# Optimization experiments

Hardware: AMD Instinct MI355X
Metric: run time of the kernel (lower is better)

Reference implementation:

```python
import jax, jax.numpy as jnp
import numpy as np

B, S, D, E, L = 4, 384, 300, 50, 2
HD = D // L  # head_dim = 150


def _linear_params(k, fin, fout):
    bnd = 1.0 / np.sqrt(fin)
    kw, kb = jax.random.split(k)
    W = jax.random.uniform(kw, (fout, fin), minval=-bnd, maxval=bnd, dtype=jnp.float32)
    b = jax.random.uniform(kb, (fout,), minval=-bnd, maxval=bnd, dtype=jnp.float32)
    return W, b


def setup_inputs() -> dict:
    key = jax.random.key(0)
    ks = jax.random.split(key, 6)
    W0, b0 = _linear_params(ks[0], D, HD)            # weight_list[0]: Linear(300, 150)
    W1, b1 = _linear_params(ks[1], D + HD, HD)       # weight_list[1]: Linear(450, 150)
    Wh, bh = _linear_params(ks[2], 2 * HD + E, E)    # Edgeupdate.W: Linear(350, 50)
    Wout, bout = _linear_params(ks[3], D, D)         # linear_output: Linear(300, 300)
    adj = jax.random.uniform(ks[4], (B, S, S, E), dtype=jnp.float32)
    gcn_inputs = jax.random.normal(ks[5], (B, S, D), dtype=jnp.float32)
    return dict(adj=adj, gcn_inputs=gcn_inputs, W0=W0, b0=b0, W1=W1, b1=b1,
                Wh=Wh, bh=bh, Wout=Wout, bout=bout)


def reference(adj, gcn_inputs, W0, b0, W1, b1, Wh, bh, Wout, bout):
    # Edgeupdate weight split: cat order is [edge(E), node1(HD), node2(HD)]
    Wh_e = Wh[:, :E]            # [E, E]
    Wh_1 = Wh[:, E:E + HD]      # [E, HD]
    Wh_2 = Wh[:, E + HD:]       # [E, HD]

    outputs = gcn_inputs        # [B, S, D]
    cache = [gcn_inputs]
    out_list = []
    for (Wl, bl) in ((W0, b0), (W1, b1)):
        e_dim = adj.shape[-1]
        # mean over edge channels of (adj_e @ outputs): einsum fuses the mean
        Ax = jnp.einsum('bike,bkd->bid', adj, outputs) / e_dim   # [B, S, din]
        # AxW = W_l(Ax) + W_l(outputs)  (same linear applied twice, bias twice)
        AxW = (Ax @ Wl.T + bl) + (outputs @ Wl.T + bl)           # [B, S, HD]
        gAxW = jax.nn.relu(AxW)
        # Edgeupdate highway: new_edge[b,i,j] = W([edge[b,i,j]; g[b,j]; g[b,i]]) + bh
        # (node1[b,i,j] = g[b,j], node2[b,i,j] = g[b,i] from the expand/permute)
        edge_part = adj @ Wh_e.T                                  # [B, S, S, E]
        n1 = gAxW @ Wh_1.T                                        # [B, S, E]
        n2 = gAxW @ Wh_2.T                                        # [B, S, E]
        adj = edge_part + n1[:, None, :, :] + n2[:, :, None, :] + bh
        cache.append(gAxW)
        outputs = jnp.concatenate(cache, axis=2)                  # growing concat
        out_list.append(gAxW)  # gcn_drop is identity in eval mode

    gcn_outputs = jnp.concatenate(out_list, axis=2) + gcn_inputs  # [B, S, D]
    return gcn_outputs @ Wout.T + bout
```

## Files before the change

### kernel.cpp

```cpp
#include <hip/hip_runtime.h>

constexpr int Bc  = 4;
constexpr int Sc  = 384;
constexpr int Dc  = 300;
constexpr int Ec  = 50;
constexpr int HDc = 150;
constexpr int WHC = 350;
constexpr int MT  = Bc * Sc;

typedef __attribute__((ext_vector_type(8))) short bf16x8;
typedef __attribute__((ext_vector_type(4))) float f32x4;

__device__ __forceinline__ short f2bf(float x) {
    union { float f; unsigned u; } v; v.f = x;
    unsigned r = (v.u + 0x7FFFu + ((v.u >> 16) & 1u)) >> 16;
    return (short)r;
}

__device__ __forceinline__ void s12_unit(const float* __restrict__ G,
                                         const float* __restrict__ sm,
                                         float* __restrict__ s12, int unit)
{
    int wave = threadIdx.x >> 6, lane = threadIdx.x & 63;
    int g = unit * 4 + wave;
    const float* gp = G + (long)g * Dc;
    float a = 0.f, c = 0.f;
    #pragma unroll
    for (int h0 = 0; h0 < HDc; h0 += 64) {
        int h = h0 + lane;
        if (h < HDc) { float v = gp[h]; a += v * sm[64 + h]; c += v * sm[224 + h]; }
    }
    #pragma unroll
    for (int off = 32; off; off >>= 1) {
        a += __shfl_down(a, off);
        c += __shfl_down(c, off);
    }
    if (lane == 0) { s12[2*g] = a; s12[2*g + 1] = c; }
}

template<int BSRC, int A1M, int HASD, int HASB, int RELU, int PRE>
__device__ __forceinline__ void mgemm_body(
    short* As, short* Bs, int bx, int by, int b,
    const float* __restrict__ A, int lda, long sA,
    const float* __restrict__ Bw, int ldb, long sB,
    const float* __restrict__ W1a, const float* __restrict__ WoutP,
    const float* __restrict__ Dm, int ldd, long sD,
    const float* __restrict__ bias, float bscale,
    const float* __restrict__ s12, const float* __restrict__ sm,
    float* __restrict__ C, int ldc, long sC,
    int M, int N, int K)
{
    const float* Ap = A + (long)b * sA;
    const float* Bp = Bw + (long)b * sB;
    const float* Dp = Dm + (long)b * sD;
    float* Cp = C + (long)b * sC;

    const int tid  = threadIdx.x;
    const int wave = tid >> 6, lane = tid & 63;
    const int wm = wave & 1, wn = wave >> 1;
    const int lm = lane & 15, quad = lane >> 4;
    const int m0 = by * 32, n0 = bx * 32;

    const int srow = tid >> 3;
    const int sk   = (tid & 7) * 8;
    const int nc   = tid & 31;
    const int kr   = tid >> 5;

    float sbh = 0.f; const float* s1p = nullptr; float s2v = 0.f;
    if constexpr (A1M) {
        sbh = sm[384];
        s1p = s12 + 2L * Sc * b;
        s2v = s1p[2 * (m0 + srow) + 1];
    }

    const int cn = n0 + wn * 16 + lm;
    float bpre = 0.f;
    float dpre[4] = {0.f, 0.f, 0.f, 0.f};
    if constexpr (PRE) {
        if constexpr (HASB) { if (cn < N) bpre = bias[cn]; }
        if constexpr (HASD) {
            #pragma unroll
            for (int r = 0; r < 4; ++r) {
                int cm = m0 + wm * 16 + quad * 4 + r;
                if (cn < N && cm < M) dpre[r] = Dp[(long)cm * ldd + cn];
            }
        }
    }

    float ra[8], rb[8];

    auto stageA = [&](int k0) {
        int am = m0 + srow;
        int kb = k0 + sk;
        if constexpr (A1M) {
            float4 u = *(const float4*)(Ap + (long)am * lda + kb);
            float4 w = *(const float4*)(Ap + (long)am * lda + kb + 4);
            const float* up = (const float*)&u;
            const float* wp = (const float*)&w;
            #pragma unroll
            for (int j = 0; j < 4; ++j) {
                ra[j]     = (up[j] + s1p[2*(kb + j)]     + s2v + sbh) * (1.0f/Ec);
                ra[4 + j] = (wp[j] + s1p[2*(kb + 4 + j)] + s2v + sbh) * (1.0f/Ec);
            }
        } else {
            if (kb + 7 < K) {
                float4 u = *(const float4*)(Ap + (long)am * lda + kb);
                float4 w = *(const float4*)(Ap + (long)am * lda + kb + 4);
                ra[0]=u.x; ra[1]=u.y; ra[2]=u.z; ra[3]=u.w;
                ra[4]=w.x; ra[5]=w.y; ra[6]=w.z; ra[7]=w.w;
            } else {
                #pragma unroll
                for (int j = 0; j < 8; ++j) {
                    int k = kb + j;
                    ra[j] = (k < K) ? Ap[(long)am * lda + k] : 0.f;
                }
            }
        }
    };

    auto stageB = [&](int k0) {
        if constexpr (BSRC == 0) {
            int n = n0 + nc;
            bool nok = n < N;
            #pragma unroll
            for (int p = 0; p < 8; ++p) {
                int k = k0 + kr + p * 8;
                rb[p] = nok ? Bp[(long)k * ldb + n] : 0.f;
            }
        } else {
            int nr = n0 + srow;
            bool nok = nr < N;
            const float* wp = Bp; int ld = ldb; int nn = nr;
            if constexpr (BSRC == 2) {
                if (nr < 150)      { wp = Bp;    ld = 300; nn = nr; }
                else if (nr < 300) { wp = W1a;   ld = 450; nn = nr - 150; }
                else               { wp = WoutP; ld = 300; nn = nr - 300; }
            }
            #pragma unroll
            for (int p = 0; p < 4; ++p) {
                int k = k0 + sk + 2 * p;
                if (nok && k + 1 < K) {
                    float2 v = *(const float2*)(wp + (long)nn * ld + k);
                    rb[2*p] = v.x; rb[2*p + 1] = v.y;
                } else {
                    rb[2*p]     = (nok && k < K)     ? wp[(long)nn * ld + k]     : 0.f;
                    rb[2*p + 1] = (nok && k + 1 < K) ? wp[(long)nn * ld + k + 1] : 0.f;
                }
            }
        }
    };

    auto stash = [&]() {
        #pragma unroll
        for (int j = 0; j < 8; ++j) As[srow * 72 + sk + j] = f2bf(ra[j]);
        if constexpr (BSRC == 0) {
            #pragma unroll
            for (int p = 0; p < 8; ++p) Bs[nc * 72 + kr + p * 8] = f2bf(rb[p]);
        } else {
            #pragma unroll
            for (int j = 0; j < 8; ++j) Bs[srow * 72 + sk + j] = f2bf(rb[j]);
        }
    };

    f32x4 acc = {0.f, 0.f, 0.f, 0.f};

    stageA(0); stageB(0);
    for (int k0 = 0; k0 < K; k0 += 64) {
        __syncthreads();
        stash();
        __syncthreads();
        if (k0 + 64 < K) { stageA(k0 + 64); stageB(k0 + 64); }
        {
            bf16x8 a0 = *(const bf16x8*)(As + (wm*16 + lm) * 72 + quad * 8);
            bf16x8 b0 = *(const bf16x8*)(Bs + (wn*16 + lm) * 72 + quad * 8);
            acc = __builtin_amdgcn_mfma_f32_16x16x32_bf16(a0, b0, acc, 0, 0, 0);
            bf16x8 a1 = *(const bf16x8*)(As + (wm*16 + lm) * 72 + 32 + quad * 8);
            bf16x8 b1 = *(const bf16x8*)(Bs + (wn*16 + lm) * 72 + 32 + quad * 8);
            acc = __builtin_amdgcn_mfma_f32_16x16x32_bf16(a1, b1, acc, 0, 0, 0);
        }
    }

    if (cn < N) {
        #pragma unroll
        for (int r = 0; r < 4; ++r) {
            int cm = m0 + wm * 16 + quad * 4 + r;
            if (cm < M) {
                float v = acc[r];
                if constexpr (HASD) v += PRE ? dpre[r] : Dp[(long)cm * ldd + cn];
                if constexpr (HASB) v += bscale * (PRE ? bpre : bias[cn]);
                if constexpr (RELU) v = fmaxf(v, 0.f);
                Cp[(long)cm * ldc + cn] = v;
            }
        }
    }
}

template<int BSRC, int A1M, int HASD, int HASB, int RELU>
__global__ __launch_bounds__(256)
void mgemm(const float* __restrict__ A, int lda, long sA,
           const float* __restrict__ Bw, int ldb, long sB,
           const float* __restrict__ W1a, const float* __restrict__ WoutP,
           const float* __restrict__ Dm, int ldd, long sD,
           const float* __restrict__ bias, float bscale,
           const float* __restrict__ s12, const float* __restrict__ sm,
           float* __restrict__ C, int ldc, long sC,
           int M, int N, int K)
{
    __shared__ short As[32 * 72];
    __shared__ short Bs[32 * 72];
    mgemm_body<BSRC,A1M,HASD,HASB,RELU,1>(As, Bs,
        blockIdx.x, blockIdx.y, blockIdx.z,
        A, lda, sA, Bw, ldb, sB, W1a, WoutP, Dm, ldd, sD,
        bias, bscale, s12, sm, C, ldc, sC, M, N, K);
}

__global__ __launch_bounds__(256)
void fused1(const float* __restrict__ adj, const float* __restrict__ X,
            const float* __restrict__ W0, const float* __restrict__ W1,
            const float* __restrict__ Wout, const float* __restrict__ Wh,
            const float* __restrict__ bh,
            float* __restrict__ sm, float* __restrict__ A0,
            float* __restrict__ wadj, float* __restrict__ R)
{
    __shared__ float lds[64 * 51 + 64];
    const int bx = blockIdx.x, t = threadIdx.x;

    if (bx < 912) {
        short* As = (short*)lds;
        short* Bs = As + 32 * 72;
        mgemm_body<2,0,0,0,0,0>(As, Bs, bx % 19, bx / 19, 0,
            X, Dc, 0, W0, 300, 0, W1, Wout,
            nullptr, 0, 0, nullptr, 0.f, nullptr, nullptr,
            R, 600, 0, MT, 600, Dc);
    } else if (bx == 912) {
        for (int u = t; u < 512; u += 256) {
            if (u < Ec) {
                float s = 0.f;
                for (int e = 0; e < Ec; ++e) s += Wh[e*WHC + u];
                sm[u] = s;
            } else if (u >= 64 && u < 64 + HDc) {
                int h = u - 64; float s = 0.f;
                for (int e = 0; e < Ec; ++e) s += Wh[e*WHC + Ec + h];
                sm[u] = s;
            } else if (u >= 224 && u < 224 + HDc) {
                int h = u - 224; float s = 0.f;
                for (int e = 0; e < Ec; ++e) s += Wh[e*WHC + Ec + HDc + h];
                sm[u] = s;
            } else if (u == 384) {
                float s = 0.f;
                for (int e = 0; e < Ec; ++e) s += bh[e];
                sm[u] = s;
            }
        }
    } else {
        const int unit = bx - 913;
        float* tile = lds;
        float* wec  = lds + 64 * 51;

        long base = (long)unit * 3200;
        const float4* p4 = (const float4*)(adj + base);
        float4 v0 = p4[t];
        float4 v1 = p4[t + 256];
        float4 v2 = p4[t + 512];
        float4 v3 = {0.f, 0.f, 0.f, 0.f};
        if (t < 32) v3 = p4[t + 768];

        if (t < Ec) {
            float s = 0.f;
            for (int e = 0; e < Ec; ++e) s += Wh[e * WHC + t];
            wec[t] = s;
        }

        auto scat = [&](int i, const float4& v) {
            const float* vp = (const float*)&v;
            #pragma unroll
            for (int j = 0; j < 4; ++j) {
                int e = 4 * i + j;
                tile[(e / 50) * 51 + (e % 50)] = vp[j];
            }
        };
        scat(t, v0);
        scat(t + 256, v1);
        scat(t + 512, v2);
        if (t < 32) scat(t + 768, v3);
        __syncthreads();

        int r = t >> 2, q = t & 3;
        int h0 = q * 13, h1 = (q == 3) ? 50 : h0 + 13;
        const float* row = tile + r * 51;
        float s = 0.f, w = 0.f;
        for (int i = h0; i < h1; ++i) { float v = row[i]; s += v; w += v * wec[i]; }
        s += __shfl_xor(s, 1); w += __shfl_xor(w, 1);
        s += __shfl_xor(s, 2); w += __shfl_xor(w, 2);
        if (q == 0) {
            int g = unit * 64 + r;
            A0[g]   = s * (1.0f / Ec);
            wadj[g] = w;
        }
    }
}

__global__ __launch_bounds__(256)
void fused3(const float* __restrict__ Gbuf, const float* __restrict__ sm,
            float* __restrict__ s12, const float* __restrict__ W1,
            float* __restrict__ R, const float* __restrict__ Wout,
            const float* __restrict__ bout, float* __restrict__ out)
{
    __shared__ short As[32 * 72];
    __shared__ short Bs[32 * 72];
    const int bx = blockIdx.x;

    if (bx < 480) {
        mgemm_body<1,0,1,1,0,1>(As, Bs, bx % 10, bx / 10, 0,
            Gbuf, Dc, 0, Wout, Dc, 0, nullptr, nullptr,
            R + 2 * HDc, 600, 0, bout, 1.0f, nullptr, nullptr,
            out, Dc, 0, MT, Dc, HDc);
    } else if (bx < 480 + 240) {
        int v = bx - 480;
        mgemm_body<1,0,1,0,0,1>(As, Bs, v % 5, v / 5, 0,
            Gbuf, Dc, 0, W1 + Dc, Dc + HDc, 0, nullptr, nullptr,
            R + HDc, 600, 0, nullptr, 0.f, nullptr, nullptr,
            R + HDc, 600, 0, MT, HDc, HDc);
    } else {
        s12_unit(Gbuf, sm, s12, bx - 720);
    }
}

extern "C" void kernel_launch(void* const* d_in, const int* in_sizes, int n_in,
                              void* d_out, int out_size, void* d_ws, size_t ws_size,
                              hipStream_t stream) {
    const float* adj  = (const float*)d_in[0];
    const float* X    = (const float*)d_in[1];
    const float* W0   = (const float*)d_in[2];
    const float* b0   = (const float*)d_in[3];
    const float* W1   = (const float*)d_in[4];
    const float* b1   = (const float*)d_in[5];
    const float* Wh   = (const float*)d_in[6];
    const float* bh   = (const float*)d_in[7];
    const float* Wout = (const float*)d_in[8];
    const float* bout = (const float*)d_in[9];
    float* out = (float*)d_out;

    float* ws   = (float*)d_ws;
    float* sm   = ws;
    float* A0   = sm + 512;
    float* wadj = A0 + Bc * Sc * Sc;
    float* R    = wadj + Bc * Sc * Sc;
    float* Gbuf = R + (long)Bc * Sc * 600;
    float* s12  = Gbuf + (long)Bc * Sc * Dc;

    const long AS = (long)Sc * Sc;
    const long RS = (long)Sc * 600;
    const long GS = (long)Sc * Dc;

    fused1<<<912 + 1 + (Bc*Sc*Sc)/64, 256, 0, stream>>>(
        adj, X, W0, W1, Wout, Wh, bh, sm, A0, wadj, R);

    mgemm<0,0,1,1,1><<<dim3(5, 12, Bc), 256, 0, stream>>>(
        A0, Sc, AS, R, 600, RS, nullptr, nullptr,
        R, 600, RS, b0, 2.0f, nullptr, nullptr,
        Gbuf, Dc, GS, Sc, HDc, Sc);

    fused3<<<480 + 240 + 384, 256, 0, stream>>>(
        Gbuf, sm, s12, W1, R, Wout, bout, out);

    mgemm<0,1,1,1,1><<<dim3(5, 12, Bc), 256, 0, stream>>>(
        wadj, Sc, AS, R + HDc, 600, RS, nullptr, nullptr,
        R + HDc, 600, RS, b1, 2.0f, s12, sm,
        Gbuf + HDc, Dc, GS, Sc, HDc, Sc);

    mgemm<1,0,1,0,0><<<dim3(10, 48, 1), 256, 0, stream>>>(
        Gbuf + HDc, Dc, 0, Wout + HDc, Dc, 0, nullptr, nullptr,
        out, Dc, 0, nullptr, 0.f, nullptr, nullptr,
        out, Dc, 0, MT, Dc, HDc);
}
```

Measured before the change: 225.9 us.

## Fuse per-layer aggregation, projection and output GEMMs into row-block kernels

Replaces the four post-setup launches (two batched aggregation GEMMs, a mixed fused3 kernel, and an output GEMM) with two kernels. Each block of 32 rows runs the full layer chain in shared memory: the adjacency aggregation, then the ReLU node features kept in LDS as bf16, then the s12 edge scalars, the W1 projection and the Wout contribution. The second kernel also applies the s12/bias edge correction while staging the A tile. This removes launches and the Gbuf round trips through global memory. The cost is only 48 blocks on a many-CU GPU, heavy register and LDS use, and serial work inside each block, so low occupancy could outweigh the savings.

```diff
diff --git a/kernel.cpp b/kernel.cpp
--- a/kernel.cpp
+++ b/kernel.cpp
@@ -17,25 +17,9 @@
     return (short)r;
 }
 
-__device__ __forceinline__ void s12_unit(const float* __restrict__ G,
-                                         const float* __restrict__ sm,
-                                         float* __restrict__ s12, int unit)
-{
-    int wave = threadIdx.x >> 6, lane = threadIdx.x & 63;
-    int g = unit * 4 + wave;
-    const float* gp = G + (long)g * Dc;
-    float a = 0.f, c = 0.f;
-    #pragma unroll
-    for (int h0 = 0; h0 < HDc; h0 += 64) {
-        int h = h0 + lane;
-        if (h < HDc) { float v = gp[h]; a += v * sm[64 + h]; c += v * sm[224 + h]; }
-    }
-    #pragma unroll
-    for (int off = 32; off; off >>= 1) {
-        a += __shfl_down(a, off);
-        c += __shfl_down(c, off);
-    }
-    if (lane == 0) { s12[2*g] = a; s12[2*g + 1] = c; }
+__device__ __forceinline__ float bf2f(short s) {
+    union { unsigned u; float f; } v; v.u = ((unsigned)(unsigned short)s) << 16;
+    return v.f;
 }
 
 template<int BSRC, int A1M, int HASD, int HASB, int RELU, int PRE>
@@ -193,25 +177,6 @@
             }
         }
     }
-}
-
-template<int BSRC, int A1M, int HASD, int HASB, int RELU>
-__global__ __launch_bounds__(256)
-void mgemm(const float* __restrict__ A, int lda, long sA,
-           const float* __restrict__ Bw, int ldb, long sB,
-           const float* __restrict__ W1a, const float* __restrict__ WoutP,
-           const float* __restrict__ Dm, int ldd, long sD,
-           const float* __restrict__ bias, float bscale,
-           const float* __restrict__ s12, const float* __restrict__ sm,
-           float* __restrict__ C, int ldc, long sC,
-           int M, int N, int K)
-{
-    __shared__ short As[32 * 72];
-    __shared__ short Bs[32 * 72];
-    mgemm_body<BSRC,A1M,HASD,HASB,RELU,1>(As, Bs,
-        blockIdx.x, blockIdx.y, blockIdx.z,
-        A, lda, sA, Bw, ldb, sB, W1a, WoutP, Dm, ldd, sD,
-        bias, bscale, s12, sm, C, ldc, sC, M, N, K);
 }
 
 __global__ __launch_bounds__(256)
@@ -301,28 +266,368 @@
 }
 
 __global__ __launch_bounds__(256)
-void fused3(const float* __restrict__ Gbuf, const float* __restrict__ sm,
-            float* __restrict__ s12, const float* __restrict__ W1,
-            float* __restrict__ R, const float* __restrict__ Wout,
-            const float* __restrict__ bout, float* __restrict__ out)
+void fused23(const float* __restrict__ A0, float* __restrict__ R,
+             const float* __restrict__ W1, const float* __restrict__ Wout,
+             const float* __restrict__ b0v, const float* __restrict__ boutv,
+             const float* __restrict__ smv, float* __restrict__ s12,
+             float* __restrict__ out)
 {
-    __shared__ short As[32 * 72];
-    __shared__ short Bs[32 * 72];
-    const int bx = blockIdx.x;
-
-    if (bx < 480) {
-        mgemm_body<1,0,1,1,0,1>(As, Bs, bx % 10, bx / 10, 0,
-            Gbuf, Dc, 0, Wout, Dc, 0, nullptr, nullptr,
-            R + 2 * HDc, 600, 0, bout, 1.0f, nullptr, nullptr,
-            out, Dc, 0, MT, Dc, HDc);
-    } else if (bx < 480 + 240) {
-        int v = bx - 480;
-        mgemm_body<1,0,1,0,0,1>(As, Bs, v % 5, v / 5, 0,
-            Gbuf, Dc, 0, W1 + Dc, Dc + HDc, 0, nullptr, nullptr,
-            R + HDc, 600, 0, nullptr, 0.f, nullptr, nullptr,
-            R + HDc, 600, 0, MT, HDc, HDc);
-    } else {
-        s12_unit(Gbuf, sm, s12, bx - 720);
+    __shared__ short A6[6 * 2304];
+    __shared__ short Bs5[5 * 2304];
+    __shared__ short Gs[3 * 2304];
+
+    const int tid  = threadIdx.x;
+    const int wave = tid >> 6, lane = tid & 63;
+    const int wm = wave & 1, wn = wave >> 1;
+    const int lm = lane & 15, quad = lane >> 4;
+    const int srow = tid >> 3, sk = (tid & 7) * 8;
+    const int nc = tid & 31, kr = tid >> 5;
+    const int cml = wm * 16 + quad * 4;
+
+    const int b  = blockIdx.x / 12;
+    const int m0 = (blockIdx.x % 12) * 32;
+    const int gm0 = b * Sc + m0;
+    const float* Ap = A0 + (long)b * (Sc * Sc);
+    const float* Pp = R  + (long)b * (Sc * 600);
+
+    for (int i = tid; i < 3 * 2304; i += 256) Gs[i] = 0;
+
+    #pragma unroll
+    for (int c = 0; c < 6; ++c) {
+        const float* ap = Ap + (long)(m0 + srow) * Sc + c * 64 + sk;
+        float4 u = *(const float4*)ap;
+        float4 w = *(const float4*)(ap + 4);
+        short* d = A6 + c * 2304 + srow * 72 + sk;
+        d[0]=f2bf(u.x); d[1]=f2bf(u.y); d[2]=f2bf(u.z); d[3]=f2bf(u.w);
+        d[4]=f2bf(w.x); d[5]=f2bf(w.y); d[6]=f2bf(w.z); d[7]=f2bf(w.w);
+    }
+
+    float dpre[5][4], b0pre[5];
+    #pragma unroll
+    for (int nt = 0; nt < 5; ++nt) {
+        int cn = nt * 32 + wn * 16 + lm;
+        b0pre[nt] = (cn < 150) ? b0v[cn] : 0.f;
+        #pragma unroll
+        for (int r = 0; r < 4; ++r)
+            dpre[nt][r] = (cn < 150) ? Pp[(long)(m0 + cml + r) * 600 + cn] : 0.f;
+    }
+
+    float rbs[5][8];
+    f32x4 acc[5];
+    const f32x4 fz = {0.f, 0.f, 0.f, 0.f};
+
+    auto stageB_P = [&](int k0) {
+        #pragma unroll
+        for (int nt = 0; nt < 5; ++nt) {
+            int n = nt * 32 + nc; bool nok = n < 150;
+            #pragma unroll
+            for (int p = 0; p < 8; ++p)
+                rbs[nt][p] = nok ? Pp[(long)(k0 + kr + p * 8) * 600 + n] : 0.f;
+        }
+    };
+    auto stashB_k = [&]() {
+        #pragma unroll
+        for (int nt = 0; nt < 5; ++nt)
+            #pragma unroll
+            for (int p = 0; p < 8; ++p)
+                Bs5[nt * 2304 + nc * 72 + kr + p * 8] = f2bf(rbs[nt][p]);
+    };
+    auto stageB_W = [&](const float* Wbase, int ldw, int nbase, int nlim,
+                        int klim, int k0) {
+        #pragma unroll
+        for (int nt = 0; nt < 5; ++nt) {
+            int nr = nbase + nt * 32 + srow; bool nok = nr < nlim;
+            const float* wp = Wbase + (long)nr * ldw;
+            #pragma unroll
+            for (int p = 0; p < 4; ++p) {
+                int k = k0 + sk + 2 * p;
+                rbs[nt][2*p]   = (nok && k     < klim) ? wp[k]     : 0.f;
+                rbs[nt][2*p+1] = (nok && k + 1 < klim) ? wp[k + 1] : 0.f;
+            }
+        }
+    };
+    auto stashB_r = [&]() {
+        #pragma unroll
+        for (int nt = 0; nt < 5; ++nt)
+            #pragma unroll
+            for (int j = 0; j < 8; ++j)
+                Bs5[nt * 2304 + srow * 72 + sk + j] = f2bf(rbs[nt][j]);
+    };
+    auto mfma5 = [&](const short* Abase, int ki) {
+        const short* Af = Abase + ki * 2304 + (wm * 16 + lm) * 72;
+        bf16x8 a0 = *(const bf16x8*)(Af + quad * 8);
+        bf16x8 a1 = *(const bf16x8*)(Af + 32 + quad * 8);
+        #pragma unroll
+        for (int nt = 0; nt < 5; ++nt) {
+            const short* Bf = Bs5 + nt * 2304 + (wn * 16 + lm) * 72;
+            acc[nt] = __builtin_amdgcn_mfma_f32_16x16x32_bf16(
+                a0, *(const bf16x8*)(Bf + quad * 8), acc[nt], 0, 0, 0);
+            acc[nt] = __builtin_amdgcn_mfma_f32_16x16x32_bf16(
+                a1, *(const bf16x8*)(Bf + 32 + quad * 8), acc[nt], 0, 0, 0);
+        }
+    };
+
+    #pragma unroll
+    for (int nt = 0; nt < 5; ++nt) acc[nt] = fz;
+    stageB_P(0);
+    for (int ki = 0; ki < 6; ++ki) {
+        __syncthreads();
+        stashB_k();
+        __syncthreads();
+        if (ki < 5) stageB_P((ki + 1) * 64);
+        mfma5(A6, ki);
+    }
+    #pragma unroll
+    for (int nt = 0; nt < 5; ++nt) {
+        int cn = nt * 32 + wn * 16 + lm;
+        if (cn < 150) {
+            #pragma unroll
+            for (int r = 0; r < 4; ++r) {
+                float g = fmaxf(acc[nt][r] + dpre[nt][r] + 2.f * b0pre[nt], 0.f);
+                Gs[(cn >> 6) * 2304 + (cml + r) * 72 + (cn & 63)] = f2bf(g);
+            }
+        }
+    }
+    __syncthreads();
+
+    float dq[5][4];
+    #pragma unroll
+    for (int nt = 0; nt < 5; ++nt) {
+        int cn = nt * 32 + wn * 16 + lm;
+        #pragma unroll
+        for (int r = 0; r < 4; ++r)
+            dq[nt][r] = (cn < 150) ? Pp[(long)(m0 + cml + r) * 600 + 150 + cn] : 0.f;
+    }
+
+    {
+        int row = tid >> 3, p = tid & 7;
+        int c0 = p * 19, c1 = (c0 + 19 < 150) ? c0 + 19 : 150;
+        float a = 0.f, c2 = 0.f;
+        for (int c = c0; c < c1; ++c) {
+            float g = bf2f(Gs[(c >> 6) * 2304 + row * 72 + (c & 63)]);
+            a  += g * smv[64 + c];
+            c2 += g * smv[224 + c];
+        }
+        a += __shfl_xor(a, 1);  c2 += __shfl_xor(c2, 1);
+        a += __shfl_xor(a, 2);  c2 += __shfl_xor(c2, 2);
+        a += __shfl_xor(a, 4);  c2 += __shfl_xor(c2, 4);
+        if (p == 0) { s12[2 * (gm0 + row)] = a; s12[2 * (gm0 + row) + 1] = c2; }
+    }
+
+    #pragma unroll
+    for (int nt = 0; nt < 5; ++nt) acc[nt] = fz;
+    stageB_W(W1 + Dc, 450, 0, 150, 150, 0);
+    for (int ki = 0; ki < 3; ++ki) {
+        __syncthreads();
+        stashB_r();
+        __syncthreads();
+        if (ki < 2) stageB_W(W1 + Dc, 450, 0, 150, 150, (ki + 1) * 64);
+        mfma5(Gs, ki);
+    }
+    #pragma unroll
+    for (int nt = 0; nt < 5; ++nt) {
+        int cn = nt * 32 + wn * 16 + lm;
+        if (cn < 150) {
+            #pragma unroll
+            for (int r = 0; r < 4; ++r)
+                R[(long)(gm0 + cml + r) * 600 + 150 + cn] = acc[nt][r] + dq[nt][r];
+        }
+    }
+
+    #pragma unroll
+    for (int g = 0; g < 2; ++g) {
+        float d3[5][4], bop[5];
+        #pragma unroll
+        for (int nt = 0; nt < 5; ++nt) {
+            int cn = (g * 5 + nt) * 32 + wn * 16 + lm;
+            bop[nt] = (cn < 300) ? boutv[cn] : 0.f;
+            #pragma unroll
+            for (int r = 0; r < 4; ++r)
+                d3[nt][r] = (cn < 300) ? R[(long)(gm0 + cml + r) * 600 + 300 + cn] : 0.f;
+        }
+        #pragma unroll
+        for (int nt = 0; nt < 5; ++nt) acc[nt] = fz;
+        stageB_W(Wout, 300, g * 160, 300, 150, 0);
+        for (int ki = 0; ki < 3; ++ki) {
+            __syncthreads();
+            stashB_r();
+            __syncthreads();
+            if (ki < 2) stageB_W(Wout, 300, g * 160, 300, 150, (ki + 1) * 64);
+            mfma5(Gs, ki);
+        }
+        #pragma unroll
+        for (int nt = 0; nt < 5; ++nt) {
+            int cn = (g * 5 + nt) * 32 + wn * 16 + lm;
+            if (cn < 300) {
+                #pragma unroll
+                for (int r = 0; r < 4; ++r)
+                    out[(long)(gm0 + cml + r) * 300 + cn] = acc[nt][r] + d3[nt][r] + bop[nt];
+            }
+        }
+    }
+}
+
+__global__ __launch_bounds__(256)
+void fused45(const float* __restrict__ wadj, float* __restrict__ R,
+             const float* __restrict__ b1v, const float* __restrict__ Wout,
+             const float* __restrict__ smv, const float* __restrict__ s12v,
+             float* __restrict__ out)
+{
+    __shared__ short A6[6 * 2304];
+    __shared__ short Bs5[5 * 2304];
+    __shared__ short Gs[3 * 2304];
+
+    const int tid  = threadIdx.x;
+    const int wave = tid >> 6, lane = tid & 63;
+    const int wm = wave & 1, wn = wave >> 1;
+    const int lm = lane & 15, quad = lane >> 4;
+    const int srow = tid >> 3, sk = (tid & 7) * 8;
+    const int nc = tid & 31, kr = tid >> 5;
+    const int cml = wm * 16 + quad * 4;
+
+    const int b  = blockIdx.x / 12;
+    const int m0 = (blockIdx.x % 12) * 32;
+    const int gm0 = b * Sc + m0;
+    const float* Ap = wadj + (long)b * (Sc * Sc);
+    const float* Pp = R    + (long)b * (Sc * 600);
+
+    for (int i = tid; i < 3 * 2304; i += 256) Gs[i] = 0;
+
+    const float sbh = smv[384];
+    const float* s1p = s12v + 2L * Sc * b;
+    const float s2v = s1p[2 * (m0 + srow) + 1];
+    #pragma unroll
+    for (int c = 0; c < 6; ++c) {
+        int kb = c * 64 + sk;
+        const float* ap = Ap + (long)(m0 + srow) * Sc + kb;
+        float4 u = *(const float4*)ap;
+        float4 w = *(const float4*)(ap + 4);
+        const float* up = (const float*)&u;
+        const float* wp = (const float*)&w;
+        short* d = A6 + c * 2304 + srow * 72 + sk;
+        #pragma unroll
+        for (int j = 0; j < 4; ++j) {
+            d[j]     = f2bf((up[j] + s1p[2*(kb + j)]     + s2v + sbh) * (1.0f/Ec));
+            d[4 + j] = f2bf((wp[j] + s1p[2*(kb + 4 + j)] + s2v + sbh) * (1.0f/Ec));
+        }
+    }
+
+    float dpre[5][4], b1pre[5];
+    #pragma unroll
+    for (int nt = 0; nt < 5; ++nt) {
+        int cn = nt * 32 + wn * 16 + lm;
+        b1pre[nt] = (cn < 150) ? b1v[cn] : 0.f;
+        #pragma unroll
+        for (int r = 0; r < 4; ++r)
+            dpre[nt][r] = (cn < 150) ? Pp[(long)(m0 + cml + r) * 600 + 150 + cn] : 0.f;
+    }
+
+    float rbs[5][8];
+    f32x4 acc[5];
+    const f32x4 fz = {0.f, 0.f, 0.f, 0.f};
+
+    auto stageB_P = [&](int k0) {
+        #pragma unroll
+        for (int nt = 0; nt < 5; ++nt) {
+            int n = nt * 32 + nc; bool nok = n < 150;
+            #pragma unroll
+            for (int p = 0; p < 8; ++p)
+                rbs[nt][p] = nok ? Pp[(long)(k0 + kr + p * 8) * 600 + 150 + n] : 0.f;
+        }
+    };
+    auto stashB_k = [&]() {
+        #pragma unroll
+        for (int nt = 0; nt < 5; ++nt)
+            #pragma unroll
+            for (int p = 0; p < 8; ++p)
+                Bs5[nt * 2304 + nc * 72 + kr + p * 8] = f2bf(rbs[nt][p]);
+    };
+    auto stageB_W = [&](int nbase, int k0) {
+        #pragma unroll
+        for (int nt = 0; nt < 5; ++nt) {
+            int nr = nbase + nt * 32 + srow; bool nok = nr < 300;
+            const float* wp = Wout + (long)nr * 300 + 150;
+            #pragma unroll
+            for (int p = 0; p < 4; ++p) {
+                int k = k0 + sk + 2 * p;
+                rbs[nt][2*p]   = (nok && k     < 150) ? wp[k]     : 0.f;
+                rbs[nt][2*p+1] = (nok && k + 1 < 150) ? wp[k + 1] : 0.f;
+            }
+        }
+    };
+    auto stashB_r = [&]() {
+        #pragma unroll
+        for (int nt = 0; nt < 5; ++nt)
+            #pragma unroll
+            for (int j = 0; j < 8; ++j)
+                Bs5[nt * 2304 + srow * 72 + sk + j] = f2bf(rbs[nt][j]);
+    };
+    auto mfma5 = [&](const short* Abase, int ki) {
+        const short* Af = Abase + ki * 2304 + (wm * 16 + lm) * 72;
+        bf16x8 a0 = *(const bf16x8*)(Af + quad * 8);
+        bf16x8 a1 = *(const bf16x8*)(Af + 32 + quad * 8);
+        #pragma unroll
+        for (int nt = 0; nt < 5; ++nt) {
+            const short* Bf = Bs5 + nt * 2304 + (wn * 16 + lm) * 72;
+            acc[nt] = __builtin_amdgcn_mfma_f32_16x16x32_bf16(
+                a0, *(const bf16x8*)(Bf + quad * 8), acc[nt], 0, 0, 0);
+            acc[nt] = __builtin_amdgcn_mfma_f32_16x16x32_bf16(
+                a1, *(const bf16x8*)(Bf + 32 + quad * 8), acc[nt], 0, 0, 0);
+        }
+    };
+
+    #pragma unroll
+    for (int nt = 0; nt < 5; ++nt) acc[nt] = fz;
+    stageB_P(0);
+    for (int ki = 0; ki < 6; ++ki) {
+        __syncthreads();
+        stashB_k();
+        __syncthreads();
+        if (ki < 5) stageB_P((ki + 1) * 64);
+        mfma5(A6, ki);
+    }
+    #pragma unroll
+    for (int nt = 0; nt < 5; ++nt) {
+        int cn = nt * 32 + wn * 16 + lm;
+        if (cn < 150) {
+            #pragma unroll
+            for (int r = 0; r < 4; ++r) {
+                float g = fmaxf(acc[nt][r] + dpre[nt][r] + 2.f * b1pre[nt], 0.f);
+                Gs[(cn >> 6) * 2304 + (cml + r) * 72 + (cn & 63)] = f2bf(g);
+            }
+        }
+    }
+    __syncthreads();
+
+    #pragma unroll
+    for (int g = 0; g < 2; ++g) {
+        float op[5][4];
+        #pragma unroll
+        for (int nt = 0; nt < 5; ++nt) {
+            int cn = (g * 5 + nt) * 32 + wn * 16 + lm;
+            #pragma unroll
+            for (int r = 0; r < 4; ++r)
+                op[nt][r] = (cn < 300) ? out[(long)(gm0 + cml + r) * 300 + cn] : 0.f;
+        }
+        #pragma unroll
+        for (int nt = 0; nt < 5; ++nt) acc[nt] = fz;
+        stageB_W(g * 160, 0);
+        for (int ki = 0; ki < 3; ++ki) {
+            __syncthreads();
+            stashB_r();
+            __syncthreads();
+            if (ki < 2) stageB_W(g * 160, (ki + 1) * 64);
+            mfma5(Gs, ki);
+        }
+        #pragma unroll
+        for (int nt = 0; nt < 5; ++nt) {
+            int cn = (g * 5 + nt) * 32 + wn * 16 + lm;
+            if (cn < 300) {
+                #pragma unroll
+                for (int r = 0; r < 4; ++r)
+                    out[(long)(gm0 + cml + r) * 300 + cn] = acc[nt][r] + op[nt][r];
+            }
+        }
     }
 }
 
@@ -349,28 +654,12 @@
     float* Gbuf = R + (long)Bc * Sc * 600;
     float* s12  = Gbuf + (long)Bc * Sc * Dc;
 
-    const long AS = (long)Sc * Sc;
-    const long RS = (long)Sc * 600;
-    const long GS = (long)Sc * Dc;
-
     fused1<<<912 + 1 + (Bc*Sc*Sc)/64, 256, 0, stream>>>(
         adj, X, W0, W1, Wout, Wh, bh, sm, A0, wadj, R);
 
-    mgemm<0,0,1,1,1><<<dim3(5, 12, Bc), 256, 0, stream>>>(
-        A0, Sc, AS, R, 600, RS, nullptr, nullptr,
-        R, 600, RS, b0, 2.0f, nullptr, nullptr,
-        Gbuf, Dc, GS, Sc, HDc, Sc);
-
-    fused3<<<480 + 240 + 384, 256, 0, stream>>>(
-        Gbuf, sm, s12, W1, R, Wout, bout, out);
-
-    mgemm<0,1,1,1,1><<<dim3(5, 12, Bc), 256, 0, stream>>>(
-        wadj, Sc, AS, R + HDc, 600, RS, nullptr, nullptr,
-        R + HDc, 600, RS, b1, 2.0f, s12, sm,
-        Gbuf + HDc, Dc, GS, Sc, HDc, Sc);
-
-    mgemm<1,0,1,0,0><<<dim3(10, 48, 1), 256, 0, stream>>>(
-        Gbuf + HDc, Dc, 0, Wout + HDc, Dc, 0, nullptr, nullptr,
-        out, Dc, 0, nullptr, 0.f, nullptr, nullptr,
-        out, Dc, 0, MT, Dc, HDc);
+    fused23<<<48, 256, 0, stream>>>(
+        A0, R, W1, Wout, b0, bout, sm, s12, out);
+
+    fused45<<<48, 256, 0, stream>>>(
+        wadj, R, b1, Wout, sm, s12, out);
 }
```

New measurement: 254.9 us. 1.13x slower.
